# Kernel tuning notes

Hardware: AMD Instinct MI355X
Metric: run time of the kernel (lower is better)

Reference implementation:

```python
import jax, jax.numpy as jnp
import numpy as np

H = 16  # n_heads

def setup_inputs() -> dict:
    key = jax.random.key(0)
    k1, k2, k3, k4 = jax.random.split(key, 4)
    B, S, D = 2, 2048, 1024
    query = jax.random.normal(k1, (B, S, D), dtype=jnp.float32)
    pos_emb = jax.random.normal(k2, (S, D), dtype=jnp.float32)
    w_qkv = jax.random.normal(k3, (D, 3 * D), dtype=jnp.float32) * (D ** -0.5)
    w_out = jax.random.normal(k4, (D, D), dtype=jnp.float32) * (D ** -0.5)
    return {"query": query, "pos_emb": pos_emb, "w_qkv": w_qkv, "w_out": w_out}

def reference(query, pos_emb, w_qkv, w_out):
    B, S, D = query.shape
    d_k = D // H
    # ape=True: pos_fn applied to input before QKV projection (additive APE)
    x = query + pos_emb[None, :, :]
    # fused QKV projection; torch view(B,S,H,3*d_k) + chunk(3,-1) == reshape(B,S,H,3,d_k)
    qkv = jnp.einsum('bsd,de->bse', x, w_qkv).reshape(B, S, H, 3, d_k)
    qkv = jnp.transpose(qkv, (0, 2, 1, 3, 4))  # [B,H,S,3,d_k]
    q, k, v = qkv[..., 0, :], qkv[..., 1, :], qkv[..., 2, :]
    scale = d_k ** -0.5
    scores = jnp.einsum('bhqd,bhkd->bhqk', q, k) * scale  # [B,H,S,S]
    attn = jax.nn.softmax(scores, axis=-1)  # dropout is identity in eval
    o = jnp.einsum('bhqk,bhkd->bhqd', attn, v)
    o = jnp.transpose(o, (0, 2, 1, 3)).reshape(B, S, D)
    return jnp.einsum('bsd,de->bse', o, w_out)
```

## Files before the change

### kernel.cpp

```cpp
#include <hip/hip_runtime.h>

#define SS 2048
#define DD 1024
#define N3 3072

typedef unsigned short u16;
typedef unsigned int u32;
typedef __attribute__((ext_vector_type(8))) short bf16x8;
typedef __attribute__((ext_vector_type(4))) float f32x4;

__device__ __forceinline__ u16 f2bf(float f) {
    u32 u = __float_as_uint(f);
    u32 r = u + 0x7fffu + ((u >> 16) & 1u);
    return (u16)(r >> 16);
}

__device__ __forceinline__ float fast_exp2(float x) {
    return __builtin_amdgcn_exp2f(x);
}

__device__ __forceinline__ void async_cp16(u16* lds, const u16* g) {
    __builtin_amdgcn_global_load_lds((const __attribute__((address_space(1))) u32*)g,
                                     (__attribute__((address_space(3))) u32*)lds, 16, 0, 0);
}

__global__ __launch_bounds__(256)
void prep_x(const float* __restrict__ q, const float* __restrict__ pos, u16* __restrict__ x)
{
    const size_t i = ((size_t)blockIdx.x * 256 + threadIdx.x) * 4;
    float4 a = *(const float4*)(q + i);
    float4 p = *(const float4*)(pos + (i & (size_t)(SS * DD - 1)));
    uint2 r;
    r.x = (u32)f2bf(a.x + p.x) | ((u32)f2bf(a.y + p.y) << 16);
    r.y = (u32)f2bf(a.z + p.z) | ((u32)f2bf(a.w + p.w) << 16);
    *(uint2*)(x + i) = r;
}

template <int SQ>
__global__ __launch_bounds__(256)
void transpose_bf16(const float* __restrict__ W, u16* __restrict__ WT, int K, int N)
{
    __shared__ float t[32][33];
    const int tx = threadIdx.x & 31, ty = threadIdx.x >> 5;
    const int x0 = blockIdx.x * 32, y0 = blockIdx.y * 32;
#pragma unroll
    for (int i = 0; i < 4; ++i)
        t[ty + i * 8][tx] = W[(size_t)(y0 + ty + i * 8) * N + x0 + tx];
    __syncthreads();
#pragma unroll
    for (int i = 0; i < 4; ++i) {
        const int n = x0 + ty + i * 8;
        float v = t[tx][ty + i * 8];
        if (SQ && (n % 192) < 64) v *= 0.18033688f;
        WT[(size_t)n * K + y0 + tx] = f2bf(v);
    }
}

template <int OUT_BF16, int NT>
__global__ __launch_bounds__(256)
void gemm_mfma(const u16* __restrict__ A, const u16* __restrict__ BT,
               void* __restrict__ Cv, int M, int N, int K)
{
    constexpr int FR = NT / 32;
    __shared__ u16 As[128 * 64];
    __shared__ u16 Bs[NT * 64];

    const int tid = threadIdx.x;
    const int lane = tid & 63, wv = tid >> 6;
    const int quad = lane >> 4, l16 = lane & 15;
    const int m0 = blockIdx.y * 128, n0 = blockIdx.x * NT;

    const int arow = wv * 32 + (lane >> 3);
    const int pc   = lane & 7;
    const int lcA  = pc ^ (arow & 7);
    const u16* agp = A + (size_t)(m0 + arow) * K + lcA * 8;
    u16* alp = As + arow * 64 + pc * 8;

    const int brow = (NT == 128) ? (wv * 32 + (lane >> 3)) : (wv * 8 + (lane >> 3));
    const int lcB  = pc ^ (brow & 7);
    const u16* bgp = BT + (size_t)(n0 + brow) * K + lcB * 8;
    u16* blp = Bs + brow * 64 + pc * 8;

    const int moff = (wv >> 1) * 64, noff = (wv & 1) * (NT / 2);

    f32x4 acc[4][FR];
#pragma unroll
    for (int i = 0; i < 4; ++i)
#pragma unroll
        for (int j = 0; j < FR; ++j) acc[i][j] = {0.f, 0.f, 0.f, 0.f};

    const int swf = l16 & 7;

    for (int k0 = 0; k0 < K; k0 += 64) {
#pragma unroll
        for (int s = 0; s < 4; ++s)
            async_cp16(alp + s * 8 * 64, agp + (size_t)(s * 8) * K + k0);
        if constexpr (NT == 128) {
#pragma unroll
            for (int s = 0; s < 4; ++s)
                async_cp16(blp + s * 8 * 64, bgp + (size_t)(s * 8) * K + k0);
        } else {
#pragma unroll
            for (int s = 0; s < 2; ++s)
                async_cp16(blp + s * 32 * 64, bgp + (size_t)(s * 32) * K + k0);
        }
        __syncthreads();

#pragma unroll
        for (int ks = 0; ks < 2; ++ks) {
            bf16x8 af[4], bfr[FR];
#pragma unroll
            for (int t = 0; t < 4; ++t)
                af[t] = *(const bf16x8*)&As[(moff + t * 16 + l16) * 64 + (((ks * 4 + quad) ^ swf) << 3)];
#pragma unroll
            for (int t = 0; t < FR; ++t)
                bfr[t] = *(const bf16x8*)&Bs[(noff + t * 16 + l16) * 64 + (((ks * 4 + quad) ^ swf) << 3)];
#pragma unroll
            for (int mt = 0; mt < 4; ++mt)
#pragma unroll
                for (int nt = 0; nt < FR; ++nt)
                    acc[mt][nt] = __builtin_amdgcn_mfma_f32_16x16x32_bf16(af[mt], bfr[nt], acc[mt][nt], 0, 0, 0);
        }
        __syncthreads();
    }

#pragma unroll
    for (int mt = 0; mt < 4; ++mt)
#pragma unroll
        for (int r = 0; r < 4; ++r) {
            const size_t row = m0 + moff + mt * 16 + quad * 4 + r;
            if (OUT_BF16) {
                u16* cp = (u16*)Cv + row * N + n0 + noff + l16;
#pragma unroll
                for (int nt = 0; nt < FR; ++nt) cp[nt * 16] = f2bf(acc[mt][nt][r]);
            } else {
                float* cp = (float*)Cv + row * N + n0 + noff + l16;
#pragma unroll
                for (int nt = 0; nt < FR; ++nt) cp[nt * 16] = acc[mt][nt][r];
            }
        }
}

__global__ __launch_bounds__(256)
void attn_mfma(const u16* __restrict__ qkv, u16* __restrict__ o)
{
    __shared__ u16 Ks[2][64 * 64];
    __shared__ u16 Vn[2][64 * 64];
    __shared__ u16 Vt[64 * 64];
    __shared__ u16 Ps[4][32 * 64];

    const int tid = threadIdx.x;
    const int lane = tid & 63, wv = tid >> 6;
    const int quad = lane >> 4, l16 = lane & 15;
    const int bx = blockIdx.x;
    const int h = bx & 15, b = (bx >> 4) & 1, qt = bx >> 5;

    const size_t hb = (size_t)b * SS * N3 + h * 192;
    const int q0 = qt * 128 + wv * 32;
    const int sw = l16 & 7;

    bf16x8 qf[2][2];
#pragma unroll
    for (int mt = 0; mt < 2; ++mt)
#pragma unroll
        for (int ks = 0; ks < 2; ++ks)
            qf[mt][ks] = *(const bf16x8*)(qkv + hb + (size_t)(q0 + mt * 16 + l16) * N3 + ks * 32 + quad * 8);

    f32x4 po[2][4];
#pragma unroll
    for (int mt = 0; mt < 2; ++mt)
#pragma unroll
        for (int nt = 0; nt < 4; ++nt) po[mt][nt] = {0.f, 0.f, 0.f, 0.f};
    float lrun[2] = {0.f, 0.f};

    const int lrow = lane >> 3;
    const int pc8  = lane & 7;
    const int lc   = pc8 ^ lrow;
    const int srow = wv * 16;
    const u16* kgp = qkv + hb + 64  + (size_t)(srow + lrow) * N3 + lc * 8;
    const u16* vgp = kgp + 64;

    const int kp = tid & 31, dkb = (tid >> 5) * 8;

    {
        u16* kb = Ks[0] + (srow + lrow) * 64 + pc8 * 8;
        u16* vb = Vn[0] + (srow + lrow) * 64 + pc8 * 8;
        async_cp16(kb,          kgp);
        async_cp16(kb + 8 * 64, kgp + (size_t)8 * N3);
        async_cp16(vb,          vgp);
        async_cp16(vb + 8 * 64, vgp + (size_t)8 * N3);
    }

    for (int kt = 0; kt < SS / 64; ++kt) {
        const int p = kt & 1;

        if (kt < SS / 64 - 1) {
            const size_t koff = (size_t)(kt + 1) * 64 * N3;
            u16* kb = Ks[p ^ 1] + (srow + lrow) * 64 + pc8 * 8;
            u16* vb = Vn[p ^ 1] + (srow + lrow) * 64 + pc8 * 8;
            async_cp16(kb,          kgp + koff);
            async_cp16(kb + 8 * 64, kgp + koff + (size_t)8 * N3);
            async_cp16(vb,          vgp + koff);
            async_cp16(vb + 8 * 64, vgp + koff + (size_t)8 * N3);
            asm volatile("s_waitcnt vmcnt(4) lgkmcnt(0)\n\ts_barrier" ::: "memory");
        } else {
            asm volatile("s_waitcnt vmcnt(0) lgkmcnt(0)\n\ts_barrier" ::: "memory");
        }

        const u16* kbuf = Ks[p];
        const u16* vbuf = Vn[p];

        {
            uint4 a4 = *(const uint4*)&vbuf[(2 * kp)     * 64 + (((dkb >> 3) ^ ((2 * kp)     & 7)) << 3)];
            uint4 b4 = *(const uint4*)&vbuf[(2 * kp + 1) * 64 + (((dkb >> 3) ^ ((2 * kp + 1) & 7)) << 3)];
            u32 ar[4] = {a4.x, a4.y, a4.z, a4.w};
            u32 br[4] = {b4.x, b4.y, b4.z, b4.w};
#pragma unroll
            for (int j = 0; j < 8; ++j) {
                const u32 sel = (j & 1) ? 0x07060302u : 0x05040100u;
                const u32 w = __builtin_amdgcn_perm(br[j >> 1], ar[j >> 1], sel);
                const int row = dkb + j;
                *(u32*)&Vt[row * 64 + (((kp >> 2) ^ (row & 7)) << 3) + ((2 * kp) & 7)] = w;
            }
        }

        f32x4 sf[2][4];
#pragma unroll
        for (int mt = 0; mt < 2; ++mt)
#pragma unroll
            for (int kn = 0; kn < 4; ++kn) sf[mt][kn] = {0.f, 0.f, 0.f, 0.f};
        __builtin_amdgcn_s_setprio(1);
#pragma unroll
        for (int ks = 0; ks < 2; ++ks)
#pragma unroll
            for (int kn = 0; kn < 4; ++kn) {
                bf16x8 kf = *(const bf16x8*)&kbuf[(kn * 16 + l16) * 64 + (((ks * 4 + quad) ^ sw) << 3)];
#pragma unroll
                for (int mt = 0; mt < 2; ++mt)
                    sf[mt][kn] = __builtin_amdgcn_mfma_f32_16x16x32_bf16(kf, qf[mt][ks], sf[mt][kn], 0, 0, 0);
            }
        __builtin_amdgcn_s_setprio(0);

#pragma unroll
        for (int mt = 0; mt < 2; ++mt) {
            float ls = 0.f;
#pragma unroll
            for (int kn = 0; kn < 4; ++kn) {
                const float p0 = fast_exp2(sf[mt][kn][0]);
                const float p1 = fast_exp2(sf[mt][kn][1]);
                const float p2 = fast_exp2(sf[mt][kn][2]);
                const float p3 = fast_exp2(sf[mt][kn][3]);
                const u32 w0 = __builtin_amdgcn_perm(__float_as_uint(p1), __float_as_uint(p0), 0x07060302u);
                const u32 w1 = __builtin_amdgcn_perm(__float_as_uint(p3), __float_as_uint(p2), 0x07060302u);
                ls += __uint_as_float(w0 << 16) + __uint_as_float(w0 & 0xffff0000u)
                    + __uint_as_float(w1 << 16) + __uint_as_float(w1 & 0xffff0000u);
                const int ch = (2 * kn + (quad >> 1)) ^ sw;
                uint2 wp; wp.x = w0; wp.y = w1;
                *(uint2*)&Ps[wv][(mt * 16 + l16) * 64 + (ch << 3) + ((quad & 1) << 2)] = wp;
            }
            lrun[mt] += ls;
        }

        asm volatile("s_waitcnt lgkmcnt(0)\n\ts_barrier" ::: "memory");

        __builtin_amdgcn_s_setprio(1);
#pragma unroll
        for (int ks = 0; ks < 2; ++ks) {
            bf16x8 pf[2], vf[4];
#pragma unroll
            for (int mt = 0; mt < 2; ++mt)
                pf[mt] = *(const bf16x8*)&Ps[wv][(mt * 16 + l16) * 64 + (((ks * 4 + quad) ^ sw) << 3)];
#pragma unroll
            for (int nt = 0; nt < 4; ++nt)
                vf[nt] = *(const bf16x8*)&Vt[(nt * 16 + l16) * 64 + (((ks * 4 + quad) ^ sw) << 3)];
#pragma unroll
            for (int mt = 0; mt < 2; ++mt)
#pragma unroll
                for (int nt = 0; nt < 4; ++nt)
                    po[mt][nt] = __builtin_amdgcn_mfma_f32_16x16x32_bf16(pf[mt], vf[nt], po[mt][nt], 0, 0, 0);
        }
        __builtin_amdgcn_s_setprio(0);
    }

#pragma unroll
    for (int mt = 0; mt < 2; ++mt) {
        lrun[mt] += __shfl_xor(lrun[mt], 16, 64);
        lrun[mt] += __shfl_xor(lrun[mt], 32, 64);
    }
#pragma unroll
    for (int mt = 0; mt < 2; ++mt) {
        float linv[4];
#pragma unroll
        for (int r = 0; r < 4; ++r)
            linv[r] = 1.f / __shfl(lrun[mt], quad * 4 + r, 64);
#pragma unroll
        for (int r = 0; r < 4; ++r) {
            const size_t row = (size_t)b * SS + q0 + mt * 16 + quad * 4 + r;
            u16* op = o + row * DD + h * 64 + l16;
#pragma unroll
            for (int nt = 0; nt < 4; ++nt)
                op[nt * 16] = f2bf(po[mt][nt][r] * linv[r]);
        }
    }
}

extern "C" void kernel_launch(void* const* d_in, const int* in_sizes, int n_in,
                              void* d_out, int out_size, void* d_ws, size_t ws_size,
                              hipStream_t stream)
{
    const float* query  = (const float*)d_in[0];
    const float* posemb = (const float*)d_in[1];
    const float* w_qkv  = (const float*)d_in[2];
    const float* w_out  = (const float*)d_in[3];
    float* out = (float*)d_out;

    u16* xb    = (u16*)d_ws;
    u16* wqkvT = xb    + (size_t)4096 * 1024;
    u16* woutT = wqkvT + (size_t)3072 * 1024;
    u16* qkv   = woutT + (size_t)1024 * 1024;
    u16* ob    = qkv   + (size_t)4096 * 3072;

    prep_x<<<4096, 256, 0, stream>>>(query, posemb, xb);
    transpose_bf16<1><<<dim3(N3 / 32, DD / 32), 256, 0, stream>>>(w_qkv, wqkvT, DD, N3);
    transpose_bf16<0><<<dim3(DD / 32, DD / 32), 256, 0, stream>>>(w_out, woutT, DD, DD);

    gemm_mfma<1, 128><<<dim3(N3 / 128, 4096 / 128), 256, 0, stream>>>(xb, wqkvT, (void*)qkv, 4096, N3, DD);

    attn_mfma<<<dim3(512, 1, 1), 256, 0, stream>>>(qkv, ob);

    gemm_mfma<0, 64><<<dim3(DD / 64, 4096 / 128), 256, 0, stream>>>(ob, woutT, (void*)out, 4096, DD, DD);
}
```

Baseline: 201.4 us.

## Split attention KV loop across two wave groups, pre-transpose V, keep P in registers

Adds a separate kernel that writes V transposed to global memory, which removes the per-tile LDS transpose from the attention loop. The attention block grows to 512 threads: two groups of four waves each process half the key range and are combined through LDS at the end. The P tile stays in registers and feeds 16x16x16 MFMAs directly, which drops the Ps LDS round trip and a barrier. In exchange it adds a kernel launch, extra global traffic for the V transpose, and a wait of vmcnt(0) at every iteration that reduces prefetch overlap.

```diff
diff --git a/kernel.cpp b/kernel.cpp
--- a/kernel.cpp
+++ b/kernel.cpp
@@ -7,6 +7,7 @@
 typedef unsigned short u16;
 typedef unsigned int u32;
 typedef __attribute__((ext_vector_type(8))) short bf16x8;
+typedef __attribute__((ext_vector_type(4))) short bf16x4;
 typedef __attribute__((ext_vector_type(4))) float f32x4;
 
 __device__ __forceinline__ u16 f2bf(float f) {
@@ -22,6 +23,10 @@
 __device__ __forceinline__ void async_cp16(u16* lds, const u16* g) {
     __builtin_amdgcn_global_load_lds((const __attribute__((address_space(1))) u32*)g,
                                      (__attribute__((address_space(3))) u32*)lds, 16, 0, 0);
+}
+
+__device__ __forceinline__ f32x4 mfma16(bf16x4 a, bf16x4 b, f32x4 c) {
+    return __builtin_amdgcn_mfma_f32_16x16x16bf16_1k(a, b, c, 0, 0, 0);
 }
 
 __global__ __launch_bounds__(256)
@@ -56,6 +61,27 @@
     }
 }
 
+__global__ __launch_bounds__(256)
+void transpose_v(const u16* __restrict__ qkv, u16* __restrict__ vt)
+{
+    __shared__ u16 t[64][72];
+    const int bx = blockIdx.x;
+    const int bh = bx >> 5, st = bx & 31;
+    const int b = bh >> 4, h = bh & 15;
+    const int r = threadIdx.x >> 2, c16 = (threadIdx.x & 3) * 16;
+
+    const u16* src = qkv + (size_t)(b * SS + st * 64 + r) * N3 + h * 192 + 128 + c16;
+    *(uint4*)&t[r][c16]     = *(const uint4*)src;
+    *(uint4*)&t[r][c16 + 8] = *(const uint4*)(src + 8);
+    __syncthreads();
+
+    union { uint4 q[2]; u16 hh[16]; } u;
+#pragma unroll
+    for (int j = 0; j < 16; ++j) u.hh[j] = t[c16 + j][r];
+    uint4* dst = (uint4*)(vt + ((size_t)bh * 64 + r) * SS + st * 64 + c16);
+    dst[0] = u.q[0]; dst[1] = u.q[1];
+}
+
 template <int OUT_BF16, int NT>
 __global__ __launch_bounds__(256)
 void gemm_mfma(const u16* __restrict__ A, const u16* __restrict__ BT,
@@ -141,22 +167,21 @@
         }
 }
 
-__global__ __launch_bounds__(256)
-void attn_mfma(const u16* __restrict__ qkv, u16* __restrict__ o)
-{
-    __shared__ u16 Ks[2][64 * 64];
-    __shared__ u16 Vn[2][64 * 64];
-    __shared__ u16 Vt[64 * 64];
-    __shared__ u16 Ps[4][32 * 64];
+__global__ __launch_bounds__(512, 4)
+void attn_mfma(const u16* __restrict__ qkv, const u16* __restrict__ vt, u16* __restrict__ o)
+{
+    __shared__ __align__(16) u16 smem[32768];
 
     const int tid = threadIdx.x;
     const int lane = tid & 63, wv = tid >> 6;
+    const int grp = wv >> 2, w4 = wv & 3;
     const int quad = lane >> 4, l16 = lane & 15;
     const int bx = blockIdx.x;
-    const int h = bx & 15, b = (bx >> 4) & 1, qt = bx >> 5;
+    const int bh = bx & 31, qt = bx >> 5;
+    const int h = bh & 15, b = bh >> 4;
 
     const size_t hb = (size_t)b * SS * N3 + h * 192;
-    const int q0 = qt * 128 + wv * 32;
+    const int q0 = qt * 128 + w4 * 32;
     const int sw = l16 & 7;
 
     bf16x8 qf[2][2];
@@ -173,56 +198,37 @@
         for (int nt = 0; nt < 4; ++nt) po[mt][nt] = {0.f, 0.f, 0.f, 0.f};
     float lrun[2] = {0.f, 0.f};
 
-    const int lrow = lane >> 3;
-    const int pc8  = lane & 7;
-    const int lc   = pc8 ^ lrow;
-    const int srow = wv * 16;
-    const u16* kgp = qkv + hb + 64  + (size_t)(srow + lrow) * N3 + lc * 8;
-    const u16* vgp = kgp + 64;
-
-    const int kp = tid & 31, dkb = (tid >> 5) * 8;
-
-    {
-        u16* kb = Ks[0] + (srow + lrow) * 64 + pc8 * 8;
-        u16* vb = Vn[0] + (srow + lrow) * 64 + pc8 * 8;
-        async_cp16(kb,          kgp);
-        async_cp16(kb + 8 * 64, kgp + (size_t)8 * N3);
-        async_cp16(vb,          vgp);
-        async_cp16(vb + 8 * 64, vgp + (size_t)8 * N3);
-    }
-
-    for (int kt = 0; kt < SS / 64; ++kt) {
-        const int p = kt & 1;
-
-        if (kt < SS / 64 - 1) {
-            const size_t koff = (size_t)(kt + 1) * 64 * N3;
-            u16* kb = Ks[p ^ 1] + (srow + lrow) * 64 + pc8 * 8;
-            u16* vb = Vn[p ^ 1] + (srow + lrow) * 64 + pc8 * 8;
-            async_cp16(kb,          kgp + koff);
-            async_cp16(kb + 8 * 64, kgp + koff + (size_t)8 * N3);
-            async_cp16(vb,          vgp + koff);
-            async_cp16(vb + 8 * 64, vgp + koff + (size_t)8 * N3);
-            asm volatile("s_waitcnt vmcnt(4) lgkmcnt(0)\n\ts_barrier" ::: "memory");
-        } else {
-            asm volatile("s_waitcnt vmcnt(0) lgkmcnt(0)\n\ts_barrier" ::: "memory");
-        }
-
-        const u16* kbuf = Ks[p];
-        const u16* vbuf = Vn[p];
-
-        {
-            uint4 a4 = *(const uint4*)&vbuf[(2 * kp)     * 64 + (((dkb >> 3) ^ ((2 * kp)     & 7)) << 3)];
-            uint4 b4 = *(const uint4*)&vbuf[(2 * kp + 1) * 64 + (((dkb >> 3) ^ ((2 * kp + 1) & 7)) << 3)];
-            u32 ar[4] = {a4.x, a4.y, a4.z, a4.w};
-            u32 br[4] = {b4.x, b4.y, b4.z, b4.w};
-#pragma unroll
-            for (int j = 0; j < 8; ++j) {
-                const u32 sel = (j & 1) ? 0x07060302u : 0x05040100u;
-                const u32 w = __builtin_amdgcn_perm(br[j >> 1], ar[j >> 1], sel);
-                const int row = dkb + j;
-                *(u32*)&Vt[row * 64 + (((kp >> 2) ^ (row & 7)) << 3) + ((2 * kp) & 7)] = w;
-            }
-        }
+    const int lrow = lane >> 3, pc8 = lane & 7, lc = pc8 ^ lrow;
+    const int srow = w4 * 16;
+    const int kt0 = grp * 16;
+
+    const u16* kgp = qkv + hb + 64 + (size_t)(kt0 * 64 + srow + lrow) * N3 + lc * 8;
+    const u16* vgp = vt + ((size_t)bh * 64 + srow + lrow) * SS + kt0 * 64 + lc * 8;
+
+    u16* const ksA = smem + (grp * 2) * 4096 + (srow + lrow) * 64 + pc8 * 8;
+    u16* const ksB = ksA + 4096;
+    u16* const vsA = smem + 16384 + (grp * 2) * 4096 + (srow + lrow) * 64 + pc8 * 8;
+    u16* const vsB = vsA + 4096;
+
+    async_cp16(ksA,       kgp);
+    async_cp16(ksA + 512, kgp + (size_t)8 * N3);
+    async_cp16(vsA,       vgp);
+    async_cp16(vsA + 512, vgp + (size_t)8 * SS);
+
+    for (int it = 0; it < 16; ++it) {
+        const int p = it & 1;
+        asm volatile("s_waitcnt vmcnt(0) lgkmcnt(0)\n\ts_barrier" ::: "memory");
+        if (it < 15) {
+            const size_t ko = (size_t)(it + 1) * 64;
+            u16* kb = p ? ksA : ksB;
+            u16* vb = p ? vsA : vsB;
+            async_cp16(kb,       kgp + ko * N3);
+            async_cp16(kb + 512, kgp + ko * N3 + (size_t)8 * N3);
+            async_cp16(vb,       vgp + ko);
+            async_cp16(vb + 512, vgp + ko + (size_t)8 * SS);
+        }
+        const u16* kbuf = smem + (grp * 2 + p) * 4096;
+        const u16* vbuf = smem + 16384 + (grp * 2 + p) * 4096;
 
         f32x4 sf[2][4];
 #pragma unroll
@@ -241,6 +247,7 @@
             }
         __builtin_amdgcn_s_setprio(0);
 
+        u32 SW[2][4][2];
 #pragma unroll
         for (int mt = 0; mt < 2; ++mt) {
             float ls = 0.f;
@@ -254,52 +261,71 @@
                 const u32 w1 = __builtin_amdgcn_perm(__float_as_uint(p3), __float_as_uint(p2), 0x07060302u);
                 ls += __uint_as_float(w0 << 16) + __uint_as_float(w0 & 0xffff0000u)
                     + __uint_as_float(w1 << 16) + __uint_as_float(w1 & 0xffff0000u);
-                const int ch = (2 * kn + (quad >> 1)) ^ sw;
-                uint2 wp; wp.x = w0; wp.y = w1;
-                *(uint2*)&Ps[wv][(mt * 16 + l16) * 64 + (ch << 3) + ((quad & 1) << 2)] = wp;
+                SW[mt][kn][0] = w0;
+                SW[mt][kn][1] = w1;
             }
             lrun[mt] += ls;
         }
 
-        asm volatile("s_waitcnt lgkmcnt(0)\n\ts_barrier" ::: "memory");
-
         __builtin_amdgcn_s_setprio(1);
 #pragma unroll
-        for (int ks = 0; ks < 2; ++ks) {
-            bf16x8 pf[2], vf[4];
-#pragma unroll
-            for (int mt = 0; mt < 2; ++mt)
-                pf[mt] = *(const bf16x8*)&Ps[wv][(mt * 16 + l16) * 64 + (((ks * 4 + quad) ^ sw) << 3)];
+        for (int kn = 0; kn < 4; ++kn) {
+            bf16x4 vf[4];
 #pragma unroll
             for (int nt = 0; nt < 4; ++nt)
-                vf[nt] = *(const bf16x8*)&Vt[(nt * 16 + l16) * 64 + (((ks * 4 + quad) ^ sw) << 3)];
-#pragma unroll
-            for (int mt = 0; mt < 2; ++mt)
+                vf[nt] = *(const bf16x4*)&vbuf[(nt * 16 + l16) * 64 + (((2 * kn + (quad >> 1)) ^ sw) << 3) + ((quad & 1) << 2)];
+#pragma unroll
+            for (int mt = 0; mt < 2; ++mt) {
+                union { bf16x4 v; u32 w[2]; } pu;
+                pu.w[0] = SW[mt][kn][0];
+                pu.w[1] = SW[mt][kn][1];
 #pragma unroll
                 for (int nt = 0; nt < 4; ++nt)
-                    po[mt][nt] = __builtin_amdgcn_mfma_f32_16x16x32_bf16(pf[mt], vf[nt], po[mt][nt], 0, 0, 0);
+                    po[mt][nt] = mfma16(vf[nt], pu.v, po[mt][nt]);
+            }
         }
         __builtin_amdgcn_s_setprio(0);
     }
+
+    __syncthreads();
 
 #pragma unroll
     for (int mt = 0; mt < 2; ++mt) {
         lrun[mt] += __shfl_xor(lrun[mt], 16, 64);
         lrun[mt] += __shfl_xor(lrun[mt], 32, 64);
     }
-#pragma unroll
-    for (int mt = 0; mt < 2; ++mt) {
-        float linv[4];
-#pragma unroll
-        for (int r = 0; r < 4; ++r)
-            linv[r] = 1.f / __shfl(lrun[mt], quad * 4 + r, 64);
-#pragma unroll
-        for (int r = 0; r < 4; ++r) {
-            const size_t row = (size_t)b * SS + q0 + mt * 16 + quad * 4 + r;
-            u16* op = o + row * DD + h * 64 + l16;
+
+    float* xch = (float*)smem;
+    if (grp == 1) {
+        float* d = xch + (w4 * 64 + lane) * 36;
+#pragma unroll
+        for (int mt = 0; mt < 2; ++mt)
 #pragma unroll
             for (int nt = 0; nt < 4; ++nt)
-                op[nt * 16] = f2bf(po[mt][nt][r] * linv[r]);
+                *(f32x4*)(d + mt * 16 + nt * 4) = po[mt][nt];
+        d[32] = lrun[0]; d[33] = lrun[1];
+    }
+    __syncthreads();
+    if (grp == 0) {
+        const float* s = xch + (w4 * 64 + lane) * 36;
+#pragma unroll
+        for (int mt = 0; mt < 2; ++mt)
+#pragma unroll
+            for (int nt = 0; nt < 4; ++nt)
+                po[mt][nt] = po[mt][nt] + *(const f32x4*)(s + mt * 16 + nt * 4);
+        lrun[0] += s[32]; lrun[1] += s[33];
+
+#pragma unroll
+        for (int mt = 0; mt < 2; ++mt) {
+            const float linv = 1.f / lrun[mt];
+            const size_t row = (size_t)b * SS + q0 + mt * 16 + l16;
+#pragma unroll
+            for (int nt = 0; nt < 4; ++nt) {
+                const u32 h0 = (u32)f2bf(po[mt][nt][0] * linv) | ((u32)f2bf(po[mt][nt][1] * linv) << 16);
+                const u32 h1 = (u32)f2bf(po[mt][nt][2] * linv) | ((u32)f2bf(po[mt][nt][3] * linv) << 16);
+                uint2 wp; wp.x = h0; wp.y = h1;
+                *(uint2*)(o + row * DD + h * 64 + nt * 16 + quad * 4) = wp;
+            }
         }
     }
 }
@@ -319,6 +345,7 @@
     u16* woutT = wqkvT + (size_t)3072 * 1024;
     u16* qkv   = woutT + (size_t)1024 * 1024;
     u16* ob    = qkv   + (size_t)4096 * 3072;
+    u16* vtb   = ob    + (size_t)4096 * 1024;
 
     prep_x<<<4096, 256, 0, stream>>>(query, posemb, xb);
     transpose_bf16<1><<<dim3(N3 / 32, DD / 32), 256, 0, stream>>>(w_qkv, wqkvT, DD, N3);
@@ -326,7 +353,9 @@
 
     gemm_mfma<1, 128><<<dim3(N3 / 128, 4096 / 128), 256, 0, stream>>>(xb, wqkvT, (void*)qkv, 4096, N3, DD);
 
-    attn_mfma<<<dim3(512, 1, 1), 256, 0, stream>>>(qkv, ob);
+    transpose_v<<<1024, 256, 0, stream>>>(qkv, vtb);
+
+    attn_mfma<<<dim3(512, 1, 1), 512, 0, stream>>>(qkv, vtb, ob);
 
     gemm_mfma<0, 64><<<dim3(DD / 64, 4096 / 128), 256, 0, stream>>>(ob, woutT, (void*)out, 4096, DD, DD);
 }
```

After: 194.1 us. 1.04x faster.
